# Optimization experiments

Hardware: AMD Instinct MI355X
Metric: run time of the kernel (lower is better)

The kernel has to match this reference:

```python
import jax, jax.numpy as jnp
import numpy as np

B, T0, J = 32, 2048, 128
C, T_L = 512, 16


def setup_inputs() -> dict:
    key = jax.random.key(0)
    k1, k2, k3, k4, k5 = jax.random.split(key, 5)
    x = jax.random.normal(k1, (B, T0, J), dtype=jnp.float32)
    lens = jax.random.randint(k2, (B,), 0, T0 - T_L)  # ensure idx stays in-range
    sos = jax.random.normal(k3, (J,), dtype=jnp.float32)
    label_seqs = jax.random.uniform(k4, (C, T_L, J), dtype=jnp.float32)
    W = jax.random.normal(k5, (J, J), dtype=jnp.float32) / np.sqrt(J)
    return {"x": x, "lens": lens, "sos": sos, "label_seqs": label_seqs, "W": W}


def _similarity(pred_seq, labels):
    # per-neuron squared-error similarity, averaged over J: [B,Tl,J],[C,Tl,J] -> [B,C,Tl]
    p2 = jnp.sum(pred_seq * pred_seq, axis=-1)          # [B,Tl]
    l2 = jnp.sum(labels * labels, axis=-1)              # [C,Tl]
    cross = jnp.einsum('btj,ctj->bct', pred_seq, labels)
    return (p2[:, None, :] + l2[None, :, :] - 2.0 * cross) / pred_seq.shape[-1]


def reference(x, lens, sos, label_seqs, W):
    b_ar = jnp.arange(B)
    sos_b = jnp.broadcast_to(sos, (B, J))
    # place sos at position lens[b], then prepend sos (vectorized scatter)
    x = x.at[b_ar, lens].set(sos_b)
    x = jnp.concatenate([sos_b[:, None, :], x], axis=1)  # [B, T0+1, J]
    idx2d = jnp.arange(T_L)[None, :] + lens[:, None] + 1  # [B, T_l]

    def gather_pred(xc):
        pred = jnp.einsum('btj,jk->btk', xc, W)          # stub search_forward
        return pred[b_ar[:, None], idx2d]                # [B, T_l, J]

    pls = gather_pred(x)
    sim0 = _similarity(pls[:, :1, :], label_seqs[:, :1, :])  # [B,C,1]
    sofar = jnp.argmin(sim0[:, :, 0], axis=-1)               # [B]

    def body(t, carry):
        xc, sofar, _ = carry
        lab = label_seqs[sofar]                              # [B, T_l, J]
        xc = xc.at[b_ar[:, None], idx2d].set(lab)            # fused scatter update
        pls = gather_pred(xc)
        sim = _similarity(pls, label_seqs)                   # [B, C, T_l]
        mask = (jnp.arange(T_L) < t).astype(sim.dtype)
        sim_mean = jnp.sum(sim * mask, axis=-1) / t
        sofar = jnp.argmin(sim_mean, axis=-1)
        return (xc, sofar, pls)

    _, sofar, pls = jax.lax.fori_loop(1, T_L + 1, body, (x, sofar, pls))
    return sofar, pls
```

## Files before the change

### kernel.cpp

```cpp
#include <hip/hip_runtime.h>

#define Jd   128
#define Cn   512
#define TLn  16
#define Bn   32


__device__ __forceinline__ unsigned int f2ord(float f) {
    unsigned int u = __float_as_uint(f);
    return (u & 0x80000000u) ? ~u : (u | 0x80000000u);
}
__device__ __forceinline__ unsigned long long packkey(float v, int c) {
    return ((unsigned long long)f2ord(v) << 32) | (unsigned int)c;
}

__global__ void __launch_bounds__(256, 4)
k_prep3(const float* __restrict__ L, const float* __restrict__ W,
        float* __restrict__ LT, float* __restrict__ l2T,
        float* __restrict__ PLT) {
    __shared__ float Lst[128][36];
    __shared__ float Ws[128][68];
    int tid = threadIdx.x, bid = blockIdx.x;
    int tau = bid & 15, jh = (bid >> 4) & 1, c0 = (bid >> 5) * 32;
    int j0 = jh * 64;

    int cr = tid >> 3, oc = tid & 7;
    const float4* src = (const float4*)(L + ((size_t)(c0 + cr) * TLn + tau) * Jd);
    float l2p = 0.f;
    #pragma unroll
    for (int i = 0; i < 4; ++i) {
        float4 v = src[oc * 4 + i];
        int kb = (oc * 4 + i) * 4;
        Lst[kb + 0][cr] = v.x;  Lst[kb + 1][cr] = v.y;
        Lst[kb + 2][cr] = v.z;  Lst[kb + 3][cr] = v.w;
        l2p += v.x * v.x + v.y * v.y + v.z * v.z + v.w * v.w;
    }
    l2p += __shfl_down(l2p, 4, 8);
    l2p += __shfl_down(l2p, 2, 8);
    l2p += __shfl_down(l2p, 1, 8);
    if (oc == 0 && jh == 0) l2T[tau * Cn + c0 + cr] = l2p;

    #pragma unroll
    for (int r = 0; r < 8; ++r) {
        int idx = r * 256 + tid;
        int k = idx >> 4, f = idx & 15;
        *(float4*)&Ws[k][f * 4] = *(const float4*)(W + (size_t)k * Jd + j0 + f * 4);
    }
    __syncthreads();

    int c = tid & 31, jq = tid >> 5;

    if (jh == 0) {
        #pragma unroll
        for (int k = jq; k < Jd; k += 8)
            LT[((size_t)tau * Jd + k) * Cn + c0 + c] = Lst[k][c];
    }

    float acc[8] = {};
    #pragma unroll 4
    for (int k = 0; k < Jd; ++k) {
        float a = Lst[k][c];
        float4 w0 = *(const float4*)&Ws[k][jq * 8];
        float4 w1 = *(const float4*)&Ws[k][jq * 8 + 4];
        acc[0] = fmaf(a, w0.x, acc[0]);
        acc[1] = fmaf(a, w0.y, acc[1]);
        acc[2] = fmaf(a, w0.z, acc[2]);
        acc[3] = fmaf(a, w0.w, acc[3]);
        acc[4] = fmaf(a, w1.x, acc[4]);
        acc[5] = fmaf(a, w1.y, acc[5]);
        acc[6] = fmaf(a, w1.z, acc[6]);
        acc[7] = fmaf(a, w1.w, acc[7]);
    }
    #pragma unroll
    for (int i = 0; i < 8; ++i)
        PLT[((size_t)tau * Jd + j0 + jq * 8 + i) * Cn + c0 + c] = acc[i];
}

__global__ void __launch_bounds__(256, 2)
k_dot(const float* __restrict__ LT, const float* __restrict__ PLT,
      const float* __restrict__ l2T,
      const float* __restrict__ sos, const float* __restrict__ W,
      float* __restrict__ DOT, float* __restrict__ S0) {
    __shared__ float As[64][128];
    __shared__ float Bs[64][128];
    int tid = threadIdx.x, bid = blockIdx.x;

    if (bid == 256) {
        float* pred0 = &As[0][0];
        if (tid < Jd) {
            float a = 0.f;
            for (int k = 0; k < Jd; ++k) a = fmaf(sos[k], W[k * Jd + tid], a);
            pred0[tid] = a;
        }
        __syncthreads();
        float a0 = 0.f, a1 = 0.f;
        for (int jj = 0; jj < Jd; ++jj) {
            float p = pred0[jj];
            float d0 = p - LT[(size_t)jj * Cn + tid];
            float d1 = p - LT[(size_t)jj * Cn + tid + 256];
            a0 = fmaf(d0, d0, a0);
            a1 = fmaf(d1, d1, a1);
        }
        S0[tid] = a0;  S0[tid + 256] = a1;
        return;
    }

    int tau = bid & 15, st = (bid >> 4) & 3, cq = bid >> 6;
    int s0 = st * 128, c0 = cq * 128;
    int sg = tid >> 4, cg = tid & 15;

    float acc[8][8] = {};
    for (int h = 0; h < 2; ++h) {
        __syncthreads();
        const float4* Asrc = (const float4*)(PLT + ((size_t)tau * Jd + h * 64) * Cn + s0);
        #pragma unroll
        for (int i = 0; i < 8; ++i) {
            int flat = i * 256 + tid;
            int row = flat >> 5, col = flat & 31;
            *(float4*)&As[row][col * 4] = Asrc[(size_t)row * (Cn / 4) + col];
        }
        const float4* Bsrc = (const float4*)(LT + ((size_t)tau * Jd + h * 64) * Cn + c0);
        #pragma unroll
        for (int i = 0; i < 8; ++i) {
            int flat = i * 256 + tid;
            int row = flat >> 5, col = flat & 31;
            *(float4*)&Bs[row][col * 4] = Bsrc[(size_t)row * (Cn / 4) + col];
        }
        __syncthreads();
        #pragma unroll 2
        for (int j = 0; j < 64; ++j) {
            float4 a0 = *(const float4*)&As[j][sg * 4];
            float4 a1 = *(const float4*)&As[j][64 + sg * 4];
            float4 b0 = *(const float4*)&Bs[j][cg * 4];
            float4 b1 = *(const float4*)&Bs[j][64 + cg * 4];
            float av[8] = {a0.x, a0.y, a0.z, a0.w, a1.x, a1.y, a1.z, a1.w};
            float bv[8] = {b0.x, b0.y, b0.z, b0.w, b1.x, b1.y, b1.z, b1.w};
            #pragma unroll
            for (int i = 0; i < 8; ++i)
                #pragma unroll
                for (int q = 0; q < 8; ++q)
                    acc[i][q] = fmaf(av[i], bv[q], acc[i][q]);
        }
    }

    float4 l2a = *(const float4*)(l2T + tau * Cn + c0 + cg * 4);
    float4 l2b = *(const float4*)(l2T + tau * Cn + c0 + 64 + cg * 4);
    #pragma unroll
    for (int i = 0; i < 8; ++i) {
        int s = s0 + ((i < 4) ? (sg * 4 + i) : (64 + sg * 4 + (i - 4)));
        float* dst = DOT + ((size_t)s * TLn + tau) * Cn + c0;
        float4 v0 = {l2a.x - 2.f * acc[i][0], l2a.y - 2.f * acc[i][1],
                     l2a.z - 2.f * acc[i][2], l2a.w - 2.f * acc[i][3]};
        float4 v1 = {l2b.x - 2.f * acc[i][4], l2b.y - 2.f * acc[i][5],
                     l2b.z - 2.f * acc[i][6], l2b.w - 2.f * acc[i][7]};
        *(float4*)(dst + cg * 4) = v0;
        *(float4*)(dst + 64 + cg * 4) = v1;
    }
}

__global__ void k_seq(const float* __restrict__ S0, const float* __restrict__ DOT,
                      int* __restrict__ keys) {
    int lane = threadIdx.x;
    int sCur = 0;

    for (int t = 0; t <= TLn; ++t) {
        unsigned long long m;
        if (t == 0) {
            float4 v0 = *(const float4*)(S0 + lane * 4);
            float4 v1 = *(const float4*)(S0 + 256 + lane * 4);
            float v[8] = {v0.x, v0.y, v0.z, v0.w, v1.x, v1.y, v1.z, v1.w};
            m = packkey(v[0], lane * 4);
            #pragma unroll
            for (int i = 1; i < 8; ++i) {
                int c = (i < 4) ? (lane * 4 + i) : (256 + lane * 4 + (i - 4));
                unsigned long long k2 = packkey(v[i], c);
                if (k2 < m) m = k2;
            }
        } else {
            const float* base = DOT + (size_t)sCur * TLn * Cn;
            float4 s0v = {0.f, 0.f, 0.f, 0.f}, s1v = {0.f, 0.f, 0.f, 0.f};
            #pragma unroll
            for (int tau = 0; tau < TLn; ++tau) {
                float4 w0 = *(const float4*)(base + (size_t)tau * Cn + lane * 4);
                float4 w1 = *(const float4*)(base + (size_t)tau * Cn + 256 + lane * 4);
                float mk = (tau < t) ? 1.f : 0.f;
                s0v.x = fmaf(w0.x, mk, s0v.x);  s0v.y = fmaf(w0.y, mk, s0v.y);
                s0v.z = fmaf(w0.z, mk, s0v.z);  s0v.w = fmaf(w0.w, mk, s0v.w);
                s1v.x = fmaf(w1.x, mk, s1v.x);  s1v.y = fmaf(w1.y, mk, s1v.y);
                s1v.z = fmaf(w1.z, mk, s1v.z);  s1v.w = fmaf(w1.w, mk, s1v.w);
            }
            float v[8] = {s0v.x, s0v.y, s0v.z, s0v.w, s1v.x, s1v.y, s1v.z, s1v.w};
            m = packkey(v[0], lane * 4);
            #pragma unroll
            for (int i = 1; i < 8; ++i) {
                int c = (i < 4) ? (lane * 4 + i) : (256 + lane * 4 + (i - 4));
                unsigned long long k2 = packkey(v[i], c);
                if (k2 < m) m = k2;
            }
        }
        #pragma unroll
        for (int o = 32; o; o >>= 1) {
            unsigned long long o2 = __shfl_down(m, o, 64);
            if (o2 < m) m = o2;
        }
        m = __shfl(m, 0, 64);
        sCur = (int)(m & 0xFFFFFFFFull);
        if (lane == 0) keys[t] = sCur;
    }
}

__global__ void k_out(const float* __restrict__ PLT, const int* __restrict__ keys,
                      float* __restrict__ out) {
    int bt = blockIdx.x, j = threadIdx.x, tau = bt & (TLn - 1);
    int s16 = keys[TLn], s15 = keys[TLn - 1];
    out[Bn + (size_t)bt * Jd + j] = PLT[((size_t)tau * Jd + j) * Cn + s15];
    if (bt == 0 && j < Bn) out[j] = (float)s16;
}

extern "C" void kernel_launch(void* const* d_in, const int* in_sizes, int n_in,
                              void* d_out, int out_size, void* d_ws, size_t ws_size,
                              hipStream_t stream) {
    const float* sos = (const float*)d_in[2];
    const float* L   = (const float*)d_in[3];
    const float* W   = (const float*)d_in[4];
    float* out = (float*)d_out;

    const size_t l2Off  = 4096;
    const size_t pltOff = 65536;
    const size_t ltOff  = pltOff + (size_t)TLn * Jd * Cn * sizeof(float);
    const size_t dotOff = ltOff  + (size_t)TLn * Jd * Cn * sizeof(float);
    const size_t need   = dotOff + (size_t)Cn * TLn * Cn * sizeof(float);
    char* base = (ws_size >= need) ? (char*)d_ws : (char*)d_in[0];
    float* S0   = (float*)base;
    int*   keys = (int*)(base + 2048);
    float* l2T  = (float*)(base + l2Off);
    float* PLT  = (float*)(base + pltOff);
    float* LT   = (float*)(base + ltOff);
    float* DOT  = (float*)(base + dotOff);

    hipLaunchKernelGGL(k_prep3, dim3(512), dim3(256), 0, stream, L, W, LT, l2T, PLT);
    hipLaunchKernelGGL(k_dot,   dim3(257), dim3(256), 0, stream,
                       LT, PLT, l2T, sos, W, DOT, S0);
    hipLaunchKernelGGL(k_seq,   dim3(1),   dim3(64), 0, stream, S0, DOT, keys);
    hipLaunchKernelGGL(k_out,   dim3(Bn * TLn), dim3(Jd), 0, stream, PLT, keys, out);
}
```

Before: 125.7 us.

## Halve k_dot tile rows for more blocks and fuse seq/out via cooperative launch

```diff
diff --git a/kernel.cpp b/kernel.cpp
--- a/kernel.cpp
+++ b/kernel.cpp
@@ -1,4 +1,7 @@
 #include <hip/hip_runtime.h>
+#include <hip/hip_cooperative_groups.h>
+
+namespace cg = cooperative_groups;
 
 #define Jd   128
 #define Cn   512
@@ -76,16 +79,16 @@
         PLT[((size_t)tau * Jd + j0 + jq * 8 + i) * Cn + c0 + c] = acc[i];
 }
 
-__global__ void __launch_bounds__(256, 2)
+__global__ void __launch_bounds__(256, 3)
 k_dot(const float* __restrict__ LT, const float* __restrict__ PLT,
       const float* __restrict__ l2T,
       const float* __restrict__ sos, const float* __restrict__ W,
       float* __restrict__ DOT, float* __restrict__ S0) {
-    __shared__ float As[64][128];
+    __shared__ float As[64][64];
     __shared__ float Bs[64][128];
     int tid = threadIdx.x, bid = blockIdx.x;
 
-    if (bid == 256) {
+    if (bid == 512) {
         float* pred0 = &As[0][0];
         if (tid < Jd) {
             float a = 0.f;
@@ -105,18 +108,18 @@
         return;
     }
 
-    int tau = bid & 15, st = (bid >> 4) & 3, cq = bid >> 6;
-    int s0 = st * 128, c0 = cq * 128;
+    int tau = bid & 15, st = (bid >> 4) & 7, cq = bid >> 7;
+    int s0 = st * 64, c0 = cq * 128;
     int sg = tid >> 4, cg = tid & 15;
 
-    float acc[8][8] = {};
+    float acc[4][8] = {};
     for (int h = 0; h < 2; ++h) {
         __syncthreads();
         const float4* Asrc = (const float4*)(PLT + ((size_t)tau * Jd + h * 64) * Cn + s0);
         #pragma unroll
-        for (int i = 0; i < 8; ++i) {
+        for (int i = 0; i < 4; ++i) {
             int flat = i * 256 + tid;
-            int row = flat >> 5, col = flat & 31;
+            int row = flat >> 4, col = flat & 15;
             *(float4*)&As[row][col * 4] = Asrc[(size_t)row * (Cn / 4) + col];
         }
         const float4* Bsrc = (const float4*)(LT + ((size_t)tau * Jd + h * 64) * Cn + c0);
@@ -127,16 +130,15 @@
             *(float4*)&Bs[row][col * 4] = Bsrc[(size_t)row * (Cn / 4) + col];
         }
         __syncthreads();
-        #pragma unroll 2
+        #pragma unroll 4
         for (int j = 0; j < 64; ++j) {
-            float4 a0 = *(const float4*)&As[j][sg * 4];
-            float4 a1 = *(const float4*)&As[j][64 + sg * 4];
+            float4 a  = *(const float4*)&As[j][sg * 4];
             float4 b0 = *(const float4*)&Bs[j][cg * 4];
             float4 b1 = *(const float4*)&Bs[j][64 + cg * 4];
-            float av[8] = {a0.x, a0.y, a0.z, a0.w, a1.x, a1.y, a1.z, a1.w};
+            float av[4] = {a.x, a.y, a.z, a.w};
             float bv[8] = {b0.x, b0.y, b0.z, b0.w, b1.x, b1.y, b1.z, b1.w};
             #pragma unroll
-            for (int i = 0; i < 8; ++i)
+            for (int i = 0; i < 4; ++i)
                 #pragma unroll
                 for (int q = 0; q < 8; ++q)
                     acc[i][q] = fmaf(av[i], bv[q], acc[i][q]);
@@ -146,8 +148,8 @@
     float4 l2a = *(const float4*)(l2T + tau * Cn + c0 + cg * 4);
     float4 l2b = *(const float4*)(l2T + tau * Cn + c0 + 64 + cg * 4);
     #pragma unroll
-    for (int i = 0; i < 8; ++i) {
-        int s = s0 + ((i < 4) ? (sg * 4 + i) : (64 + sg * 4 + (i - 4)));
+    for (int i = 0; i < 4; ++i) {
+        int s = s0 + sg * 4 + i;
         float* dst = DOT + ((size_t)s * TLn + tau) * Cn + c0;
         float4 v0 = {l2a.x - 2.f * acc[i][0], l2a.y - 2.f * acc[i][1],
                      l2a.z - 2.f * acc[i][2], l2a.w - 2.f * acc[i][3]};
@@ -158,11 +160,11 @@
     }
 }
 
-__global__ void k_seq(const float* __restrict__ S0, const float* __restrict__ DOT,
-                      int* __restrict__ keys) {
+__device__ __forceinline__ void seq_chain(const float* __restrict__ S0,
+                                          const float* __restrict__ DOT,
+                                          int* __restrict__ keys) {
     int lane = threadIdx.x;
     int sCur = 0;
-
     for (int t = 0; t <= TLn; ++t) {
         unsigned long long m;
         if (t == 0) {
@@ -209,8 +211,27 @@
     }
 }
 
+__global__ void k_seq(const float* __restrict__ S0, const float* __restrict__ DOT,
+                      int* __restrict__ keys) {
+    seq_chain(S0, DOT, keys);
+}
 __global__ void k_out(const float* __restrict__ PLT, const int* __restrict__ keys,
                       float* __restrict__ out) {
+    int bt = blockIdx.x, j = threadIdx.x, tau = bt & (TLn - 1);
+    int s16 = keys[TLn], s15 = keys[TLn - 1];
+    out[Bn + (size_t)bt * Jd + j] = PLT[((size_t)tau * Jd + j) * Cn + s15];
+    if (bt == 0 && j < Bn) out[j] = (float)s16;
+}
+
+__global__ void k_segout(const float* __restrict__ S0, const float* __restrict__ DOT,
+                         const float* __restrict__ PLT, int* __restrict__ keys,
+                         float* __restrict__ out) {
+    if (blockIdx.x == 0 && threadIdx.x < 64) {
+        seq_chain(S0, DOT, keys);
+        __threadfence();
+    }
+    cg::this_grid().sync();
+
     int bt = blockIdx.x, j = threadIdx.x, tau = bt & (TLn - 1);
     int s16 = keys[TLn], s15 = keys[TLn - 1];
     out[Bn + (size_t)bt * Jd + j] = PLT[((size_t)tau * Jd + j) * Cn + s15];
@@ -239,8 +260,21 @@
     float* DOT  = (float*)(base + dotOff);
 
     hipLaunchKernelGGL(k_prep3, dim3(512), dim3(256), 0, stream, L, W, LT, l2T, PLT);
-    hipLaunchKernelGGL(k_dot,   dim3(257), dim3(256), 0, stream,
+    hipLaunchKernelGGL(k_dot,   dim3(513), dim3(256), 0, stream,
                        LT, PLT, l2T, sos, W, DOT, S0);
-    hipLaunchKernelGGL(k_seq,   dim3(1),   dim3(64), 0, stream, S0, DOT, keys);
-    hipLaunchKernelGGL(k_out,   dim3(Bn * TLn), dim3(Jd), 0, stream, PLT, keys, out);
-}
+
+    {
+        const float* S0c = S0;  const float* DOTc = DOT;  const float* PLTc = PLT;
+        void* args[5] = {(void*)&S0c, (void*)&DOTc, (void*)&PLTc,
+                         (void*)&keys, (void*)&out};
+        hipError_t e = hipLaunchCooperativeKernel((const void*)k_segout,
+                                                  dim3(Bn * TLn), dim3(Jd),
+                                                  args, 0, stream);
+        if (e != hipSuccess) {
+            hipLaunchKernelGGL(k_seq, dim3(1),        dim3(64), 0, stream,
+                               S0, DOT, keys);
+            hipLaunchKernelGGL(k_out, dim3(Bn * TLn), dim3(Jd), 0, stream,
+                               PLT, keys, out);
+        }
+    }
+}
```

After: 169.3 us. 1.35x slower.
